# Performance work log

Hardware: AMD Instinct MI355X
Metric: run time of the kernel (lower is better)

Reference implementation:

```python
import jax, jax.numpy as jnp
import numpy as np

B, NPIX = 8, 16384
N0T, N1T = 16384, 4096
C0, C1 = 256, 512

def _pix_idx(loc, H, W):
    # loc in [-1,1] -> nearest pixel index on HxW grid (tcformer token2map convention)
    loc = jnp.clip(loc, -1.0, 1.0)
    px = jnp.clip(jnp.round((loc[..., 0] + 1.0) * W / 2.0 - 0.5), 0, W - 1).astype(jnp.int32)
    py = jnp.clip(jnp.round((loc[..., 1] + 1.0) * H / 2.0 - 0.5), 0, H - 1).astype(jnp.int32)
    return py * W + px  # [B, N0]

def token2map(x, loc_orig, idx_agg, H, W):
    # scatter token features to a HxW map, averaging tokens landing on the same pixel
    Bb, N, C = x.shape
    N0 = loc_orig.shape[1]
    flat_hw = (_pix_idx(loc_orig, H, W) + jnp.arange(Bb)[:, None] * H * W).reshape(-1)
    feat = jnp.take_along_axis(x, idx_agg[..., None], axis=1)  # [B,N0,C]
    s = jax.ops.segment_sum(feat.reshape(Bb * N0, C), flat_hw, num_segments=Bb * H * W)
    cnt = jax.ops.segment_sum(jnp.ones((Bb * N0,), x.dtype), flat_hw, num_segments=Bb * H * W)
    out = s / (cnt[:, None] + 1e-6)
    return out.reshape(Bb, H, W, C).transpose(0, 3, 1, 2)  # [B,C,H,W]

def map2token(fmap, N, loc_orig, idx_agg, agg_weight):
    # gather map pixels at loc_orig, weighted-average into N tokens via idx_agg
    Bb, C, H, W = fmap.shape
    N0 = loc_orig.shape[1]
    idx_hw = _pix_idx(loc_orig, H, W)
    pix = jnp.take_along_axis(fmap.reshape(Bb, C, H * W).transpose(0, 2, 1), idx_hw[..., None], axis=1)  # [B,N0,C]
    flat_t = (idx_agg + jnp.arange(Bb)[:, None] * N).reshape(-1)
    num = jax.ops.segment_sum((pix * agg_weight[..., None]).reshape(Bb * N0, C), flat_t, num_segments=Bb * N)
    den = jax.ops.segment_sum(agg_weight.reshape(-1), flat_t, num_segments=Bb * N)
    return (num / (den[:, None] + 1e-6)).reshape(Bb, N, C)

def token_downup(x_s, idx_agg_s, idx_agg_t, agg_weight_t, T):
    # transfer source tokens to target token set through the shared pixel grid
    Bb, S, C = x_s.shape
    N0 = idx_agg_s.shape[1]
    feat = jnp.take_along_axis(x_s, idx_agg_s[..., None], axis=1)  # [B,N0,C]
    flat_t = (idx_agg_t + jnp.arange(Bb)[:, None] * T).reshape(-1)
    num = jax.ops.segment_sum((feat * agg_weight_t[..., None]).reshape(Bb * N0, C), flat_t, num_segments=Bb * T)
    den = jax.ops.segment_sum(agg_weight_t.reshape(-1), flat_t, num_segments=Bb * T)
    return (num / (den[:, None] + 1e-6)).reshape(Bb, T, C)

def bn(x, g, b, m, v):
    # eval-mode BatchNorm over the channel (last) dim of [B,N,C] tokens
    return (x - m) / jnp.sqrt(v + 1e-5) * g + b

def setup_inputs():
    ks = jax.random.split(jax.random.key(0), 16)
    x0 = jax.random.normal(ks[0], (B, N0T, C0), jnp.float32)
    x1 = jax.random.normal(ks[1], (B, N1T, C1), jnp.float32)
    idx_agg0 = jax.random.randint(ks[2], (B, NPIX), 0, N0T)
    idx_agg1 = jax.random.randint(ks[3], (B, NPIX), 0, N1T)
    agg_weight0 = jax.random.uniform(ks[4], (B, NPIX)) + 0.1
    agg_weight1 = jax.random.uniform(ks[5], (B, NPIX)) + 0.1
    loc_orig = jax.random.uniform(ks[6], (B, NPIX, 2)) * 2.0 - 1.0
    W01 = jax.random.normal(ks[7], (C0, C1)) * (C1 ** -0.5)
    dw_w = jax.random.normal(ks[8], (C0, 1, 3, 3)) * 0.2
    skip_w = jax.random.normal(ks[9], (C0, 1, 1, 1)) * 0.2
    conv_w = jax.random.normal(ks[10], (C1, C0, 1, 1)) * (C0 ** -0.5)
    def bnp(k, C):
        k1, k2, k3, k4 = jax.random.split(k, 4)
        return (1.0 + 0.1 * jax.random.normal(k1, (C,)), 0.1 * jax.random.normal(k2, (C,)),
                0.1 * jax.random.normal(k3, (C,)), jax.random.uniform(k4, (C,)) + 0.5)
    bn01 = bnp(ks[11], C0); bn1 = bnp(ks[12], C0); bn2 = bnp(ks[13], C1)
    return dict(x0=x0, x1=x1, idx_agg0=idx_agg0, idx_agg1=idx_agg1,
                agg_weight0=agg_weight0, agg_weight1=agg_weight1, loc_orig=loc_orig,
                W01=W01, bn01_g=bn01[0], bn01_b=bn01[1], bn01_m=bn01[2], bn01_v=bn01[3],
                dw_w=dw_w, skip_w=skip_w,
                bn1_g=bn1[0], bn1_b=bn1[1], bn1_m=bn1[2], bn1_v=bn1[3],
                conv_w=conv_w, bn2_g=bn2[0], bn2_b=bn2[1], bn2_m=bn2[2], bn2_v=bn2[3],
                H0=128, W0=128)

def reference(x0, x1, idx_agg0, idx_agg1, agg_weight0, agg_weight1, loc_orig,
              W01, bn01_g, bn01_b, bn01_m, bn01_v, dw_w, skip_w,
              bn1_g, bn1_b, bn1_m, bn1_v, conv_w, bn2_g, bn2_b, bn2_m, bn2_v, H0, W0):
    # --- out branch 0: identity + (Linear C1->C0, BN, token_downup) of branch 1 ---
    src = bn(jnp.einsum('bnc,oc->bno', x1, W01), bn01_g, bn01_b, bn01_m, bn01_v)
    out0 = jax.nn.relu(x0 + token_downup(src, idx_agg1, idx_agg0, agg_weight0, x0.shape[1]))
    # --- out branch 1: identity + TokenDownLayer(branch0 -> branch1) ---
    xm = token2map(x0, loc_orig, idx_agg0, H0, W0)          # [B,C0,H0,W0]
    xm = jax.lax.conv_general_dilated(xm, dw_w, (2, 2), ((1, 1), (1, 1)),
                                      dimension_numbers=('NCHW', 'OIHW', 'NCHW'),
                                      feature_group_count=xm.shape[1])  # dw 3x3 s2
    x_back = map2token(xm, x1.shape[1], loc_orig, idx_agg1, agg_weight1)  # [B,N1,C0]
    xd = token_downup(x0, idx_agg0, idx_agg1, agg_weight1, x1.shape[1])   # [B,N1,C0]
    xd = bn(xd * skip_w.reshape(1, 1, -1) + x_back, bn1_g, bn1_b, bn1_m, bn1_v)
    xd = bn(jnp.einsum('bnc,oc->bno', xd, conv_w.reshape(C1, C0)), bn2_g, bn2_b, bn2_m, bn2_v)
    out1 = jax.nn.relu(x1 + xd)
    return out0, out1
```

## Files before the change

kernel.cpp:

```cpp
#include <hip/hip_runtime.h>
#include <hip/hip_bf16.h>

#define Bb   8
#define NPIX 16384
#define N0T  16384
#define N1T  4096
#define C0d  256
#define C1d  512

#define NKEY_P 131072
#define NKEY_0 131072
#define NKEY_1 32768
#define NKEYS  294912
#define SCAN_BLOCKS 288

#define NZINT (NKEYS * 2 + 512)
#define NZI4  ((NZINT + 3) / 4)

typedef __attribute__((ext_vector_type(8))) short bf16x8;
typedef __attribute__((ext_vector_type(4))) float f32x4;

__device__ __forceinline__ int pix_idx(float lx, float ly, int HW) {
  lx = fminf(fmaxf(lx, -1.f), 1.f);
  ly = fminf(fmaxf(ly, -1.f), 1.f);
  float half = (float)HW * 0.5f;
  int px = (int)rintf((lx + 1.0f) * half - 0.5f);
  int py = (int)rintf((ly + 1.0f) * half - 0.5f);
  px = min(max(px, 0), HW - 1);
  py = min(max(py, 0), HW - 1);
  return py * HW + px;
}

__device__ __forceinline__ short f2bf(float f) {
  union { __hip_bfloat16 h; short s; } u;
  u.h = __float2bfloat16(f);
  return u.s;
}
__device__ __forceinline__ float bf2f(short s) {
  return __uint_as_float(((unsigned)(unsigned short)s) << 16);
}

__global__ __launch_bounds__(256) void k_zero(int4* __restrict__ p) {
  int i = blockIdx.x * 256 + threadIdx.x;
  if (i < NZI4) p[i] = int4{0, 0, 0, 0};
}

__global__ __launch_bounds__(256) void k_count(
    const int* __restrict__ idx0, const int* __restrict__ idx1,
    const float* __restrict__ loc, int* __restrict__ counts) {
  int e = blockIdx.x * 256 + threadIdx.x;
  int b = e >> 14;
  float lx = loc[2 * e + 0], ly = loc[2 * e + 1];
  int kp = b * 16384 + pix_idx(lx, ly, 128);
  int k0 = NKEY_P + b * 16384 + idx0[e];
  int k1 = NKEY_P + NKEY_0 + b * 4096 + idx1[e];
  atomicAdd(&counts[kp], 1);
  atomicAdd(&counts[k0], 1);
  atomicAdd(&counts[k1], 1);
}

__global__ __launch_bounds__(256) void k_scan_block(int* __restrict__ cnt, int* __restrict__ bsum) {
  __shared__ int s[256];
  const int tid = threadIdx.x;
  const int base = blockIdx.x * 1024 + tid * 4;
  int4 v = *reinterpret_cast<const int4*>(&cnt[base]);
  int t1 = v.x + v.y, t2 = t1 + v.z, t3 = t2 + v.w;
  s[tid] = t3;
  __syncthreads();
  for (int d = 1; d < 256; d <<= 1) {
    int add = (tid >= d) ? s[tid - d] : 0;
    __syncthreads();
    s[tid] += add;
    __syncthreads();
  }
  int excl = tid ? s[tid - 1] : 0;
  int4 o;
  o.x = excl; o.y = excl + v.x; o.z = excl + t1; o.w = excl + t2;
  *reinterpret_cast<int4*>(&cnt[base]) = o;
  if (tid == 255) bsum[blockIdx.x] = s[255];
}

__global__ __launch_bounds__(512) void k_scan_top(int* __restrict__ bsum) {
  __shared__ int s[512];
  const int tid = threadIdx.x;
  int v = (tid < SCAN_BLOCKS) ? bsum[tid] : 0;
  s[tid] = v;
  __syncthreads();
  for (int d = 1; d < 512; d <<= 1) {
    int add = (tid >= d) ? s[tid - d] : 0;
    __syncthreads();
    s[tid] += add;
    __syncthreads();
  }
  int excl = tid ? s[tid - 1] : 0;
  if (tid < SCAN_BLOCKS) bsum[tid] = excl;
}

__global__ __launch_bounds__(256) void k_scan_add(int* __restrict__ off, const int* __restrict__ bsum) {
  int add = bsum[blockIdx.x];
  const int base = blockIdx.x * 1024 + threadIdx.x * 4;
  int4 v = *reinterpret_cast<const int4*>(&off[base]);
  v.x += add; v.y += add; v.z += add; v.w += add;
  *reinterpret_cast<int4*>(&off[base]) = v;
}

__global__ __launch_bounds__(256) void k_fill(
    const int* __restrict__ idx0, const int* __restrict__ idx1,
    const float* __restrict__ w0, const float* __restrict__ w1,
    const float* __restrict__ loc, const int* __restrict__ offs,
    int* __restrict__ cursor, int* __restrict__ intA,
    int* __restrict__ intB, float* __restrict__ fW) {
  int e = blockIdx.x * 256 + threadIdx.x;
  int b = e >> 14;
  float lx = loc[2 * e + 0], ly = loc[2 * e + 1];
  int i0 = idx0[e], i1 = idx1[e];
  int kp = b * 16384 + pix_idx(lx, ly, 128);
  int k0 = NKEY_P + b * 16384 + i0;
  int k1 = NKEY_P + NKEY_0 + b * 4096 + i1;
  int pP = offs[kp] + atomicAdd(&cursor[kp], 1);
  intA[pP] = b * 16384 + i0;
  int p0 = offs[k0] + atomicAdd(&cursor[k0], 1);
  intA[p0] = b * 4096 + i1;
  fW[p0 - NKEY_P] = w0[e];
  int p1 = offs[k1] + atomicAdd(&cursor[k1], 1);
  intA[p1] = b * 4096 + pix_idx(lx, ly, 64);
  intB[p1 - (NKEY_P + NKEY_0)] = b * 16384 + i0;
  fW[p1 - NKEY_P] = w1[e];
}

__global__ __launch_bounds__(256) void k_prepw(const float* __restrict__ dww, float* __restrict__ dwT) {
  int k = blockIdx.x;
  int c = threadIdx.x;
  dwT[k * 256 + c] = dww[c * 9 + k];
}

__global__ __launch_bounds__(256) void k_conv_v4(
    const float* __restrict__ x0, const int* __restrict__ offs,
    const int* __restrict__ lens, const int* __restrict__ intA,
    const float* __restrict__ dwT, short* __restrict__ xm2) {
  int byx = blockIdx.x * 4 + (threadIdx.x >> 6);
  int lane = threadIdx.x & 63;
  int c4 = lane * 4;
  int b = byx >> 12;
  int yx = byx & 4095;
  int y = yx >> 6, x = yx & 63;
  float ax = 0.f, ay = 0.f, az = 0.f, aw = 0.f;
#pragma unroll
  for (int ky = 0; ky < 3; ++ky) {
    int iy = 2 * y - 1 + ky;
    if ((unsigned)iy >= 128u) continue;
#pragma unroll
    for (int kx = 0; kx < 3; ++kx) {
      int ix = 2 * x - 1 + kx;
      if ((unsigned)ix >= 128u) continue;
      int key = b * 16384 + iy * 128 + ix;
      int st = offs[key];
      int ln = lens[key];
      float sx = 0.f, sy = 0.f, sz = 0.f, sw = 0.f;
      for (int i = 0; i < ln; ++i) {
        int row = intA[st + i];
        float4 v = *reinterpret_cast<const float4*>(&x0[(size_t)row * C0d + c4]);
        sx += v.x; sy += v.y; sz += v.z; sw += v.w;
      }
      float inv = 1.f / ((float)ln + 1e-6f);
      float4 w = *reinterpret_cast<const float4*>(&dwT[(ky * 3 + kx) * 256 + c4]);
      ax += sx * inv * w.x; ay += sy * inv * w.y;
      az += sz * inv * w.z; aw += sw * inv * w.w;
    }
  }
  short4 o;
  o.x = f2bf(ax); o.y = f2bf(ay); o.z = f2bf(az); o.w = f2bf(aw);
  *reinterpret_cast<short4*>(&xm2[(size_t)byx * C0d + c4]) = o;
}

template <int KDIM, bool FUSE, bool ABF16, bool OBF16>
__global__ __launch_bounds__(256) void k_gemm_mfma(
    const void* __restrict__ Av, const float* __restrict__ Bw,
    const float* __restrict__ g, const float* __restrict__ beta,
    const float* __restrict__ mean, const float* __restrict__ var,
    const float* __restrict__ resid, void* __restrict__ Cv, int N) {
  __shared__ __align__(16) short Als[4][128][8];
  __shared__ __align__(16) short Bls[4][64][8];
  const int t = threadIdx.x;
  const int lane = t & 63;
  const int wave = t >> 6;
  const int wm = wave >> 1;
  const int wn = wave & 1;
  const int m0 = blockIdx.x * 128;
  const int n0 = blockIdx.y * 64;
  const int l15 = lane & 15;
  const int kb = lane >> 4;
  const int arow = t >> 1, ahalf = t & 1;
  const int brow = t >> 2, bq = t & 3;
  f32x4 acc[4][2] = {};

  for (int kt = 0; kt < KDIM; kt += 32) {
    if (ABF16) {
      const short* A = (const short*)Av;
      size_t base = (size_t)(m0 + arow) * KDIM + kt + ahalf * 16;
      bf16x8 v0 = *reinterpret_cast<const bf16x8*>(&A[base]);
      bf16x8 v1 = *reinterpret_cast<const bf16x8*>(&A[base + 8]);
      *reinterpret_cast<bf16x8*>(&Als[ahalf * 2 + 0][arow][0]) = v0;
      *reinterpret_cast<bf16x8*>(&Als[ahalf * 2 + 1][arow][0]) = v1;
    } else {
      const float* A = (const float*)Av;
      size_t base = (size_t)(m0 + arow) * KDIM + kt + ahalf * 16;
      float4 f0 = *reinterpret_cast<const float4*>(&A[base + 0]);
      float4 f1 = *reinterpret_cast<const float4*>(&A[base + 4]);
      float4 f2 = *reinterpret_cast<const float4*>(&A[base + 8]);
      float4 f3 = *reinterpret_cast<const float4*>(&A[base + 12]);
      bf16x8 v0 = { f2bf(f0.x), f2bf(f0.y), f2bf(f0.z), f2bf(f0.w),
                    f2bf(f1.x), f2bf(f1.y), f2bf(f1.z), f2bf(f1.w) };
      bf16x8 v1 = { f2bf(f2.x), f2bf(f2.y), f2bf(f2.z), f2bf(f2.w),
                    f2bf(f3.x), f2bf(f3.y), f2bf(f3.z), f2bf(f3.w) };
      *reinterpret_cast<bf16x8*>(&Als[ahalf * 2 + 0][arow][0]) = v0;
      *reinterpret_cast<bf16x8*>(&Als[ahalf * 2 + 1][arow][0]) = v1;
    }
    {
      size_t base = (size_t)(n0 + brow) * KDIM + kt + bq * 8;
      float4 g0 = *reinterpret_cast<const float4*>(&Bw[base + 0]);
      float4 g1 = *reinterpret_cast<const float4*>(&Bw[base + 4]);
      bf16x8 w = { f2bf(g0.x), f2bf(g0.y), f2bf(g0.z), f2bf(g0.w),
                   f2bf(g1.x), f2bf(g1.y), f2bf(g1.z), f2bf(g1.w) };
      *reinterpret_cast<bf16x8*>(&Bls[bq][brow][0]) = w;
    }
    __syncthreads();
    bf16x8 af[4], bfr[2];
#pragma unroll
    for (int r = 0; r < 4; ++r)
      af[r] = *reinterpret_cast<const bf16x8*>(&Als[kb][wm * 64 + r * 16 + l15][0]);
#pragma unroll
    for (int s = 0; s < 2; ++s)
      bfr[s] = *reinterpret_cast<const bf16x8*>(&Bls[kb][wn * 32 + s * 16 + l15][0]);
#pragma unroll
    for (int r = 0; r < 4; ++r)
#pragma unroll
      for (int s = 0; s < 2; ++s)
        acc[r][s] = __builtin_amdgcn_mfma_f32_16x16x32_bf16(af[r], bfr[s], acc[r][s], 0, 0, 0);
    __syncthreads();
  }

  const int r0 = (lane >> 4) * 4;
#pragma unroll
  for (int s = 0; s < 2; ++s) {
    int col = n0 + wn * 32 + s * 16 + l15;
    float sc = g[col] * rsqrtf(var[col] + 1e-5f);
    float sh = beta[col] - mean[col] * sc;
#pragma unroll
    for (int r = 0; r < 4; ++r) {
      int rowb = m0 + wm * 64 + r * 16 + r0;
#pragma unroll
      for (int j = 0; j < 4; ++j) {
        int row = rowb + j;
        float v = acc[r][s][j] * sc + sh;
        if (FUSE) {
          v += resid[(size_t)row * N + col];
          v = fmaxf(v, 0.f);
        }
        if (OBF16) ((short*)Cv)[(size_t)row * N + col] = f2bf(v);
        else       ((float*)Cv)[(size_t)row * N + col] = v;
      }
    }
  }
}

__global__ __launch_bounds__(256) void k_out0_v4(
    const short* __restrict__ srcb, const float* __restrict__ x0,
    const int* __restrict__ offs, const int* __restrict__ lens,
    const int* __restrict__ intA, const float* __restrict__ fW,
    float* __restrict__ out0) {
  int row = blockIdx.x * 4 + (threadIdx.x >> 6);
  int lane = threadIdx.x & 63;
  int c4 = lane * 4;
  int key = NKEY_P + row;
  int st = offs[key];
  int ln = lens[key];
  float ax = 0.f, ay = 0.f, az = 0.f, aw = 0.f, den = 0.f;
  for (int i = 0; i < ln; ++i) {
    int sr = intA[st + i];
    float w = fW[st + i - NKEY_P];
    short4 v = *reinterpret_cast<const short4*>(&srcb[(size_t)sr * C0d + c4]);
    ax += bf2f(v.x) * w; ay += bf2f(v.y) * w;
    az += bf2f(v.z) * w; aw += bf2f(v.w) * w;
    den += w;
  }
  float inv = 1.f / (den + 1e-6f);
  size_t o = (size_t)row * C0d + c4;
  float4 xv = *reinterpret_cast<const float4*>(&x0[o]);
  float4 r;
  r.x = fmaxf(xv.x + ax * inv, 0.f);
  r.y = fmaxf(xv.y + ay * inv, 0.f);
  r.z = fmaxf(xv.z + az * inv, 0.f);
  r.w = fmaxf(xv.w + aw * inv, 0.f);
  *reinterpret_cast<float4*>(&out0[o]) = r;
}

__global__ __launch_bounds__(256) void k_out1_pre_v4(
    const short* __restrict__ xm2, const float* __restrict__ x0,
    const int* __restrict__ offs, const int* __restrict__ lens,
    const int* __restrict__ intA, const int* __restrict__ intB,
    const float* __restrict__ fW, const float* __restrict__ skip_w,
    const float* __restrict__ g, const float* __restrict__ beta,
    const float* __restrict__ mean, const float* __restrict__ var,
    short* __restrict__ xdf) {
  int row = blockIdx.x * 4 + (threadIdx.x >> 6);
  int lane = threadIdx.x & 63;
  int c4 = lane * 4;
  int key = NKEY_P + NKEY_0 + row;
  int st = offs[key];
  int ln = lens[key];
  float bx = 0.f, by = 0.f, bz = 0.f, bw = 0.f;
  float dx = 0.f, dy = 0.f, dz = 0.f, dw = 0.f, den = 0.f;
  for (int i = 0; i < ln; ++i) {
    int pr = intA[st + i];
    int sr = intB[st + i - (NKEY_P + NKEY_0)];
    float w = fW[st + i - NKEY_P];
    short4 vb = *reinterpret_cast<const short4*>(&xm2[(size_t)pr * C0d + c4]);
    float4 vd = *reinterpret_cast<const float4*>(&x0[(size_t)sr * C0d + c4]);
    bx += bf2f(vb.x) * w; by += bf2f(vb.y) * w;
    bz += bf2f(vb.z) * w; bw += bf2f(vb.w) * w;
    dx += vd.x * w; dy += vd.y * w; dz += vd.z * w; dw += vd.w * w;
    den += w;
  }
  float inv = 1.f / (den + 1e-6f);
  float4 sk = *reinterpret_cast<const float4*>(&skip_w[c4]);
  float4 gg = *reinterpret_cast<const float4*>(&g[c4]);
  float4 bb = *reinterpret_cast<const float4*>(&beta[c4]);
  float4 mm = *reinterpret_cast<const float4*>(&mean[c4]);
  float4 vv = *reinterpret_cast<const float4*>(&var[c4]);
  float s0 = gg.x * rsqrtf(vv.x + 1e-5f), h0 = bb.x - mm.x * s0;
  float s1 = gg.y * rsqrtf(vv.y + 1e-5f), h1 = bb.y - mm.y * s1;
  float s2 = gg.z * rsqrtf(vv.z + 1e-5f), h2 = bb.z - mm.z * s2;
  float s3 = gg.w * rsqrtf(vv.w + 1e-5f), h3 = bb.w - mm.w * s3;
  short4 o;
  o.x = f2bf((dx * inv * sk.x + bx * inv) * s0 + h0);
  o.y = f2bf((dy * inv * sk.y + by * inv) * s1 + h1);
  o.z = f2bf((dz * inv * sk.z + bz * inv) * s2 + h2);
  o.w = f2bf((dw * inv * sk.w + bw * inv) * s3 + h3);
  *reinterpret_cast<short4*>(&xdf[(size_t)row * C0d + c4]) = o;
}

extern "C" void kernel_launch(void* const* d_in, const int* in_sizes, int n_in,
                              void* d_out, int out_size, void* d_ws, size_t ws_size,
                              hipStream_t stream) {
  const float* x0   = (const float*)d_in[0];
  const float* x1   = (const float*)d_in[1];
  const int*   idx0 = (const int*)d_in[2];
  const int*   idx1 = (const int*)d_in[3];
  const float* w0   = (const float*)d_in[4];
  const float* w1   = (const float*)d_in[5];
  const float* loc  = (const float*)d_in[6];
  const float* W01  = (const float*)d_in[7];
  const float* bn01_g = (const float*)d_in[8];
  const float* bn01_b = (const float*)d_in[9];
  const float* bn01_m = (const float*)d_in[10];
  const float* bn01_v = (const float*)d_in[11];
  const float* dw_w   = (const float*)d_in[12];
  const float* skip_w = (const float*)d_in[13];
  const float* bn1_g  = (const float*)d_in[14];
  const float* bn1_b  = (const float*)d_in[15];
  const float* bn1_m  = (const float*)d_in[16];
  const float* bn1_v  = (const float*)d_in[17];
  const float* conv_w = (const float*)d_in[18];
  const float* bn2_g  = (const float*)d_in[19];
  const float* bn2_b  = (const float*)d_in[20];
  const float* bn2_m  = (const float*)d_in[21];
  const float* bn2_v  = (const float*)d_in[22];

  float* out = (float*)d_out;
  float* num0 = out;
  float* out1 = out + 33554432;

  int*   counts = (int*)d_ws;
  int*   cursor = counts + NKEYS;
  int*   bsum   = cursor + NKEYS;
  int*   intA   = bsum + 512;
  int*   intB   = intA + 393216;
  float* fW     = (float*)(intB + 131072);
  float* dwT    = fW + 262144;
  short* xm2    = (short*)(dwT + 2560);
  short* srcb   = xm2 + 8388608;
  short* xdf    = srcb + 8388608;

  const int nbp = Bb * NPIX;

  k_zero<<<(NZI4 + 255) / 256, 256, 0, stream>>>((int4*)d_ws);

  k_count<<<nbp / 256, 256, 0, stream>>>(idx0, idx1, loc, counts);
  k_scan_block<<<SCAN_BLOCKS, 256, 0, stream>>>(counts, bsum);
  k_scan_top<<<1, 512, 0, stream>>>(bsum);
  k_scan_add<<<SCAN_BLOCKS, 256, 0, stream>>>(counts, bsum);
  k_fill<<<nbp / 256, 256, 0, stream>>>(idx0, idx1, w0, w1, loc, counts, cursor,
                                        intA, intB, fW);
  k_prepw<<<9, 256, 0, stream>>>(dw_w, dwT);

  k_conv_v4<<<Bb * 4096 / 4, 256, 0, stream>>>(x0, counts, cursor, intA, dwT, xm2);

  {
    dim3 grid(32768 / 128, 256 / 64);
    k_gemm_mfma<512, false, false, true><<<grid, 256, 0, stream>>>(
        (const void*)x1, W01, bn01_g, bn01_b, bn01_m, bn01_v, nullptr, (void*)srcb, 256);
  }

  k_out0_v4<<<nbp / 4, 256, 0, stream>>>(srcb, x0, counts, cursor, intA, fW, num0);

  k_out1_pre_v4<<<Bb * N1T / 4, 256, 0, stream>>>(xm2, x0, counts, cursor, intA, intB,
                                                  fW, skip_w, bn1_g, bn1_b, bn1_m, bn1_v,
                                                  xdf);

  {
    dim3 grid(32768 / 128, 512 / 64);
    k_gemm_mfma<256, true, true, false><<<grid, 256, 0, stream>>>(
        (const void*)xdf, conv_w, bn2_g, bn2_b, bn2_m, bn2_v, x1, (void*)out1, 512);
  }
}
```

Measured before the change: 326.0 us.

## Widen GEMM tiles to span full output width with 512-thread blocks

Replaces the 128x64 tiled MFMA GEMM with a template whose block covers the whole N dimension (256 or 512 columns) using 8 waves, each computing a 64x64 sub-tile. Each A row tile is then loaded and converted to bf16 once instead of once per N-block, which cuts redundant global reads of the activations. In exchange there are fewer blocks (256 and 512), more accumulator registers per thread, and larger LDS tiles, which could lower occupancy. There is still no double buffering.

```diff
diff --git a/kernel.cpp b/kernel.cpp
--- a/kernel.cpp
+++ b/kernel.cpp
@@ -173,77 +173,92 @@
   *reinterpret_cast<short4*>(&xm2[(size_t)byx * C0d + c4]) = o;
 }
 
-template <int KDIM, bool FUSE, bool ABF16, bool OBF16>
-__global__ __launch_bounds__(256) void k_gemm_mfma(
+template <int KDIM, int BM, int BN, bool FUSE, bool ABF16, bool OBF16>
+__global__ __launch_bounds__(512) void k_gemm_big(
     const void* __restrict__ Av, const float* __restrict__ Bw,
     const float* __restrict__ g, const float* __restrict__ beta,
     const float* __restrict__ mean, const float* __restrict__ var,
-    const float* __restrict__ resid, void* __restrict__ Cv, int N) {
-  __shared__ __align__(16) short Als[4][128][8];
-  __shared__ __align__(16) short Bls[4][64][8];
+    const float* __restrict__ resid, void* __restrict__ Cv) {
+  constexpr int WN = BN / 64;
+  __shared__ __align__(16) short Als[4][BM][8];
+  __shared__ __align__(16) short Bls[4][BN][8];
   const int t = threadIdx.x;
   const int lane = t & 63;
   const int wave = t >> 6;
-  const int wm = wave >> 1;
-  const int wn = wave & 1;
-  const int m0 = blockIdx.x * 128;
-  const int n0 = blockIdx.y * 64;
+  const int wm = wave / WN;
+  const int wn = wave % WN;
+  const int m0 = blockIdx.x * BM;
   const int l15 = lane & 15;
   const int kb = lane >> 4;
-  const int arow = t >> 1, ahalf = t & 1;
-  const int brow = t >> 2, bq = t & 3;
-  f32x4 acc[4][2] = {};
+  f32x4 acc[4][4] = {};
 
   for (int kt = 0; kt < KDIM; kt += 32) {
-    if (ABF16) {
+    constexpr int EA = BM * 32 / 512;
+    if constexpr (ABF16) {
       const short* A = (const short*)Av;
-      size_t base = (size_t)(m0 + arow) * KDIM + kt + ahalf * 16;
-      bf16x8 v0 = *reinterpret_cast<const bf16x8*>(&A[base]);
-      bf16x8 v1 = *reinterpret_cast<const bf16x8*>(&A[base + 8]);
-      *reinterpret_cast<bf16x8*>(&Als[ahalf * 2 + 0][arow][0]) = v0;
-      *reinterpret_cast<bf16x8*>(&Als[ahalf * 2 + 1][arow][0]) = v1;
+      if constexpr (EA == 8) {
+        int row = t >> 2, koff = (t & 3) * 8;
+        bf16x8 v = *reinterpret_cast<const bf16x8*>(&A[(size_t)(m0 + row) * KDIM + kt + koff]);
+        *reinterpret_cast<bf16x8*>(&Als[koff >> 3][row][0]) = v;
+      } else {
+        int row = t >> 3, koff = (t & 7) * 4;
+        short4 v = *reinterpret_cast<const short4*>(&A[(size_t)(m0 + row) * KDIM + kt + koff]);
+        *reinterpret_cast<short4*>(&Als[koff >> 3][row][koff & 7]) = v;
+      }
     } else {
       const float* A = (const float*)Av;
-      size_t base = (size_t)(m0 + arow) * KDIM + kt + ahalf * 16;
-      float4 f0 = *reinterpret_cast<const float4*>(&A[base + 0]);
-      float4 f1 = *reinterpret_cast<const float4*>(&A[base + 4]);
-      float4 f2 = *reinterpret_cast<const float4*>(&A[base + 8]);
-      float4 f3 = *reinterpret_cast<const float4*>(&A[base + 12]);
-      bf16x8 v0 = { f2bf(f0.x), f2bf(f0.y), f2bf(f0.z), f2bf(f0.w),
-                    f2bf(f1.x), f2bf(f1.y), f2bf(f1.z), f2bf(f1.w) };
-      bf16x8 v1 = { f2bf(f2.x), f2bf(f2.y), f2bf(f2.z), f2bf(f2.w),
-                    f2bf(f3.x), f2bf(f3.y), f2bf(f3.z), f2bf(f3.w) };
-      *reinterpret_cast<bf16x8*>(&Als[ahalf * 2 + 0][arow][0]) = v0;
-      *reinterpret_cast<bf16x8*>(&Als[ahalf * 2 + 1][arow][0]) = v1;
+      if constexpr (EA == 8) {
+        int row = t >> 2, koff = (t & 3) * 8;
+        size_t base = (size_t)(m0 + row) * KDIM + kt + koff;
+        float4 f0 = *reinterpret_cast<const float4*>(&A[base]);
+        float4 f1 = *reinterpret_cast<const float4*>(&A[base + 4]);
+        bf16x8 v = { f2bf(f0.x), f2bf(f0.y), f2bf(f0.z), f2bf(f0.w),
+                     f2bf(f1.x), f2bf(f1.y), f2bf(f1.z), f2bf(f1.w) };
+        *reinterpret_cast<bf16x8*>(&Als[koff >> 3][row][0]) = v;
+      } else {
+        int row = t >> 3, koff = (t & 7) * 4;
+        size_t base = (size_t)(m0 + row) * KDIM + kt + koff;
+        float4 f = *reinterpret_cast<const float4*>(&A[base]);
+        short4 v = { f2bf(f.x), f2bf(f.y), f2bf(f.z), f2bf(f.w) };
+        *reinterpret_cast<short4*>(&Als[koff >> 3][row][koff & 7]) = v;
+      }
     }
     {
-      size_t base = (size_t)(n0 + brow) * KDIM + kt + bq * 8;
-      float4 g0 = *reinterpret_cast<const float4*>(&Bw[base + 0]);
-      float4 g1 = *reinterpret_cast<const float4*>(&Bw[base + 4]);
-      bf16x8 w = { f2bf(g0.x), f2bf(g0.y), f2bf(g0.z), f2bf(g0.w),
-                   f2bf(g1.x), f2bf(g1.y), f2bf(g1.z), f2bf(g1.w) };
-      *reinterpret_cast<bf16x8*>(&Bls[bq][brow][0]) = w;
+      constexpr int EB = BN * 32 / 512;
+      int row, koff0;
+      if constexpr (EB == 16) { row = t >> 1; koff0 = (t & 1) * 16; }
+      else                    { row = t;      koff0 = 0; }
+#pragma unroll
+      for (int c = 0; c < EB; c += 8) {
+        int koff = koff0 + c;
+        size_t base = (size_t)row * KDIM + kt + koff;
+        float4 g0 = *reinterpret_cast<const float4*>(&Bw[base]);
+        float4 g1 = *reinterpret_cast<const float4*>(&Bw[base + 4]);
+        bf16x8 w = { f2bf(g0.x), f2bf(g0.y), f2bf(g0.z), f2bf(g0.w),
+                     f2bf(g1.x), f2bf(g1.y), f2bf(g1.z), f2bf(g1.w) };
+        *reinterpret_cast<bf16x8*>(&Bls[koff >> 3][row][0]) = w;
+      }
     }
     __syncthreads();
-    bf16x8 af[4], bfr[2];
+    bf16x8 af[4], bfr[4];
 #pragma unroll
     for (int r = 0; r < 4; ++r)
       af[r] = *reinterpret_cast<const bf16x8*>(&Als[kb][wm * 64 + r * 16 + l15][0]);
 #pragma unroll
-    for (int s = 0; s < 2; ++s)
-      bfr[s] = *reinterpret_cast<const bf16x8*>(&Bls[kb][wn * 32 + s * 16 + l15][0]);
+    for (int s = 0; s < 4; ++s)
+      bfr[s] = *reinterpret_cast<const bf16x8*>(&Bls[kb][wn * 64 + s * 16 + l15][0]);
 #pragma unroll
     for (int r = 0; r < 4; ++r)
 #pragma unroll
-      for (int s = 0; s < 2; ++s)
+      for (int s = 0; s < 4; ++s)
         acc[r][s] = __builtin_amdgcn_mfma_f32_16x16x32_bf16(af[r], bfr[s], acc[r][s], 0, 0, 0);
     __syncthreads();
   }
 
   const int r0 = (lane >> 4) * 4;
 #pragma unroll
-  for (int s = 0; s < 2; ++s) {
-    int col = n0 + wn * 32 + s * 16 + l15;
+  for (int s = 0; s < 4; ++s) {
+    int col = wn * 64 + s * 16 + l15;
     float sc = g[col] * rsqrtf(var[col] + 1e-5f);
     float sh = beta[col] - mean[col] * sc;
 #pragma unroll
@@ -254,11 +269,11 @@
         int row = rowb + j;
         float v = acc[r][s][j] * sc + sh;
         if (FUSE) {
-          v += resid[(size_t)row * N + col];
+          v += resid[(size_t)row * BN + col];
           v = fmaxf(v, 0.f);
         }
-        if (OBF16) ((short*)Cv)[(size_t)row * N + col] = f2bf(v);
-        else       ((float*)Cv)[(size_t)row * N + col] = v;
+        if (OBF16) ((short*)Cv)[(size_t)row * BN + col] = f2bf(v);
+        else       ((float*)Cv)[(size_t)row * BN + col] = v;
       }
     }
   }
@@ -396,11 +411,8 @@
 
   k_conv_v4<<<Bb * 4096 / 4, 256, 0, stream>>>(x0, counts, cursor, intA, dwT, xm2);
 
-  {
-    dim3 grid(32768 / 128, 256 / 64);
-    k_gemm_mfma<512, false, false, true><<<grid, 256, 0, stream>>>(
-        (const void*)x1, W01, bn01_g, bn01_b, bn01_m, bn01_v, nullptr, (void*)srcb, 256);
-  }
+  k_gemm_big<512, 128, 256, false, false, true><<<32768 / 128, 512, 0, stream>>>(
+      (const void*)x1, W01, bn01_g, bn01_b, bn01_m, bn01_v, nullptr, (void*)srcb);
 
   k_out0_v4<<<nbp / 4, 256, 0, stream>>>(srcb, x0, counts, cursor, intA, fW, num0);
 
@@ -408,9 +420,6 @@
                                                   fW, skip_w, bn1_g, bn1_b, bn1_m, bn1_v,
                                                   xdf);
 
-  {
-    dim3 grid(32768 / 128, 512 / 64);
-    k_gemm_mfma<256, true, true, false><<<grid, 256, 0, stream>>>(
-        (const void*)xdf, conv_w, bn2_g, bn2_b, bn2_m, bn2_v, x1, (void*)out1, 512);
-  }
-}
+  k_gemm_big<256, 64, 512, true, true, false><<<32768 / 64, 512, 0, stream>>>(
+      (const void*)xdf, conv_w, bn2_g, bn2_b, bn2_m, bn2_v, x1, (void*)out1);
+}
```

Result: slower. 363.5 us (+11.5%).
